# Kernel tuning notes

Measured on AMD Instinct MI355X. Metric: run time of the kernel, lower is better.

## Reference

```python
import jax, jax.numpy as jnp
import numpy as np
from jax.ops import segment_sum

N, E, F_IN, G, C = 20000, 640000, 128, 64, 2


def setup_inputs() -> dict:
    key = jax.random.key(0)
    ks = jax.random.split(key, 16)
    g = lambda k, s: (jax.random.normal(k, s, jnp.float32) * 0.05)
    z = lambda s: jnp.zeros(s, jnp.float32)
    inp = {
        'x': jax.random.normal(ks[0], (N, F_IN), jnp.float32),
        'edge_index': jax.random.randint(ks[1], (2, E), 0, N),
        'batch': jnp.sort(jax.random.randint(ks[2], (N,), 0, G)),
        'w1': g(ks[3], (F_IN, 64)), 'b1': z((64,)),
        'w2': g(ks[4], (64, 64)), 'b2': z((64,)),
        'w3': g(ks[5], (64, 128)), 'b3': z((128,)),
        'w4': g(ks[6], (128, 256)), 'b4': z((256,)),
        'lstm_wih': g(ks[7], (512, 256)), 'lstm_whh': g(ks[8], (512, 128)),
        'lstm_bih': z((512,)), 'lstm_bhh': z((512,)),
        'attn_in_w': g(ks[9], (384, 128)), 'attn_in_b': z((384,)),
        'attn_out_w': g(ks[10], (128, 128)), 'attn_out_b': z((128,)),
        'lin1_w': g(ks[11], (64, 128)), 'lin1_b': z((64,)),
        'lin2_w': g(ks[12], (C, 64)), 'lin2_b': z((C,)),
    }
    return inp


def _gcn(x, src, dst, norm, w, b):
    # PyG GCNConv: h = x @ W; out[dst] += norm_e * h[src]; + bias
    h = x @ w
    msg = h[src] * norm[:, None]
    return segment_sum(msg, dst, num_segments=N) + b


def forward(x, edge_index, batch, w1, b1, w2, b2, w3, b3, w4, b4,
            lstm_wih, lstm_whh, lstm_bih, lstm_bhh,
            attn_in_w, attn_in_b, attn_out_w, attn_out_b,
            lin1_w, lin1_b, lin2_w, lin2_b):
    # ---- GCN normalization with self-loops (shared across layers) ----
    loop = jnp.arange(N)
    src = jnp.concatenate([edge_index[0], loop])
    dst = jnp.concatenate([edge_index[1], loop])
    deg = segment_sum(jnp.ones_like(src, jnp.float32), dst, num_segments=N)
    dinv = jnp.where(deg > 0, jax.lax.rsqrt(deg), 0.0)
    norm = dinv[src] * dinv[dst]

    h = jax.nn.relu(_gcn(x, src, dst, norm, w1, b1))   # [N,64]  (dropout = eval no-op)
    h = jax.nn.relu(_gcn(h, src, dst, norm, w2, b2))   # [N,64]
    h = jax.nn.relu(_gcn(h, src, dst, norm, w3, b3))   # [N,128]
    h = jax.nn.relu(_gcn(h, src, dst, norm, w4, b4))   # [N,256]

    # ---- LSTM over the node sequence (batch 1, seq N), PyTorch gate order i,f,g,o ----
    xg = h @ lstm_wih.T + (lstm_bih + lstm_bhh)        # [N,512] precomputed input gates

    def step(carry, xg_t):
        hh, cc = carry
        gates = xg_t + lstm_whh @ hh                    # [512]
        i, f, gg, o = jnp.split(gates, 4)
        i, f, o = jax.nn.sigmoid(i), jax.nn.sigmoid(f), jax.nn.sigmoid(o)
        cc = f * cc + i * jnp.tanh(gg)
        hh = o * jnp.tanh(cc)
        return (hh, cc), hh

    init = (jnp.zeros(128, h.dtype), jnp.zeros(128, h.dtype))
    _, hs = jax.lax.scan(step, init, xg)               # [N,128]

    # ---- MultiheadAttention: input (L=1, B=N, E=128); softmax over length-1 seq ----
    qkv = hs @ attn_in_w.T + attn_in_b                 # [N,384]
    q, k, v = jnp.split(qkv, 3, axis=-1)
    qh = q.reshape(N, 8, 16); kh = k.reshape(N, 8, 16); vh = v.reshape(N, 8, 16)
    scores = jnp.sum(qh * kh, -1, keepdims=True) / 4.0  # [N,8,1], key dim = 1
    a = jax.nn.softmax(scores, axis=-1)                 # == 1 (single key)
    ctx = (a * vh).reshape(N, 128)
    attn = ctx @ attn_out_w.T + attn_out_b             # [N,128]

    # ---- global mean pool over graphs ----
    sums = segment_sum(attn, batch, num_segments=G)    # [G,128]
    cnt = segment_sum(jnp.ones(N, attn.dtype), batch, num_segments=G)
    pooled = sums / jnp.maximum(cnt, 1.0)[:, None]

    z1 = jax.nn.relu(pooled @ lin1_w.T + lin1_b)
    logits = z1 @ lin2_w.T + lin2_b                    # [G,C]
    return jax.nn.log_softmax(logits, axis=1)


def reference(x, edge_index, batch, w1, b1, w2, b2, w3, b3, w4, b4,
              lstm_wih, lstm_whh, lstm_bih, lstm_bhh,
              attn_in_w, attn_in_b, attn_out_w, attn_out_b,
              lin1_w, lin1_b, lin2_w, lin2_b):
    return forward(x, edge_index, batch, w1, b1, w2, b2, w3, b3, w4, b4,
                   lstm_wih, lstm_whh, lstm_bih, lstm_bhh,
                   attn_in_w, attn_in_b, attn_out_w, attn_out_b,
                   lin1_w, lin1_b, lin2_w, lin2_b)
```

## Files before the change

### kernel.cpp

```cpp
#include <hip/hip_runtime.h>
#include <cstdint>
#include <cstddef>

#define N_NODES 20000
#define N_EDGES 640000
#define N_GRAPH 64

typedef __attribute__((ext_vector_type(8))) short bf16x8;
typedef __attribute__((ext_vector_type(4))) float f32x4;

__device__ __forceinline__ float sigmoidf_(float x) {
    return 1.0f / (1.0f + __expf(-x));
}
__device__ __forceinline__ float tanhf_(float x) {
    float xc = fminf(fmaxf(x, -9.0f), 9.0f);
    float e = __expf(2.0f * xc);
    return (e - 1.0f) / (e + 1.0f);
}
__device__ __forceinline__ unsigned short f2bf_(float x) {
    unsigned int u = __builtin_bit_cast(unsigned int, x);
    return (unsigned short)((u + 0x7fffu + ((u >> 16) & 1u)) >> 16);
}
__device__ __forceinline__ float sel4_(f32x4 v, bool b1, bool b2) {
    float lo = b1 ? v.y : v.x;
    float hi = b1 ? v.w : v.z;
    return b2 ? hi : lo;
}

__global__ void count_kernel(const int* __restrict__ dst, int* __restrict__ cnt, int e) {
    int i = blockIdx.x * blockDim.x + threadIdx.x;
    if (i < e) atomicAdd(&cnt[dst[i]], 1);
}

__global__ void scan_kernel(const int* __restrict__ cnt, int* __restrict__ rowstart, int n) {
    __shared__ int buf[1024];
    __shared__ int carry_sh;
    int tid = threadIdx.x;
    if (tid == 0) carry_sh = 0;
    __syncthreads();
    for (int base = 0; base < n; base += 1024) {
        int i = base + tid;
        int v = (i < n) ? cnt[i] : 0;
        buf[tid] = v;
        __syncthreads();
        for (int off = 1; off < 1024; off <<= 1) {
            int t = (tid >= off) ? buf[tid - off] : 0;
            __syncthreads();
            buf[tid] += t;
            __syncthreads();
        }
        int carry = carry_sh;
        if (i < n) rowstart[i] = carry + buf[tid] - v;
        __syncthreads();
        if (tid == 1023) carry_sh = carry + buf[1023];
        __syncthreads();
    }
    if (tid == 0) rowstart[n] = carry_sh;
}

__global__ void dinv_kernel(const int* __restrict__ cnt, float* __restrict__ dinv, int n) {
    int i = blockIdx.x * blockDim.x + threadIdx.x;
    if (i < n) dinv[i] = rsqrtf((float)cnt[i] + 1.0f);
}

__global__ void fill_kernel(const int* __restrict__ src, const int* __restrict__ dst,
                            const int* __restrict__ rowstart, int* __restrict__ cursor,
                            int* __restrict__ csr_src, int e) {
    int i = blockIdx.x * blockDim.x + threadIdx.x;
    if (i < e) {
        int d = dst[i];
        int pos = rowstart[d] + atomicAdd(&cursor[d], 1);
        csr_src[pos] = src[i];
    }
}

template <bool BT, bool RELU, bool BIAS>
__global__ void gemm_kernel(const float* __restrict__ A, const float* __restrict__ B,
                            const float* __restrict__ bias, float* __restrict__ C,
                            int M, int K, int F) {
    __shared__ float As[16][65];
    __shared__ float Bs[16][65];
    int bm = blockIdx.x * 64;
    int bn = blockIdx.y * 64;
    int tid = threadIdx.x;
    int tm = (tid >> 4) << 2;
    int tn = (tid & 15) << 2;
    float acc[4][4] = {};
    for (int k0 = 0; k0 < K; k0 += 16) {
        {
            int idx = tid * 4;
            int m = idx >> 4;
            int kk = idx & 15;
            int gm = bm + m;
            float4 v = make_float4(0.f, 0.f, 0.f, 0.f);
            if (gm < M) v = *(const float4*)&A[(size_t)gm * K + k0 + kk];
            As[kk + 0][m] = v.x; As[kk + 1][m] = v.y; As[kk + 2][m] = v.z; As[kk + 3][m] = v.w;
        }
        if (BT) {
            int idx = tid * 4;
            int nn = idx >> 4;
            int kk = idx & 15;
            float4 v = *(const float4*)&B[(size_t)(bn + nn) * K + k0 + kk];
            Bs[kk + 0][nn] = v.x; Bs[kk + 1][nn] = v.y; Bs[kk + 2][nn] = v.z; Bs[kk + 3][nn] = v.w;
        } else {
            int idx = tid * 4;
            int kk = idx >> 6;
            int nn = idx & 63;
            float4 v = *(const float4*)&B[(size_t)(k0 + kk) * F + bn + nn];
            Bs[kk][nn + 0] = v.x; Bs[kk][nn + 1] = v.y; Bs[kk][nn + 2] = v.z; Bs[kk][nn + 3] = v.w;
        }
        __syncthreads();
#pragma unroll
        for (int kk = 0; kk < 16; ++kk) {
            float av[4], bv[4];
#pragma unroll
            for (int i = 0; i < 4; ++i) av[i] = As[kk][tm + i];
#pragma unroll
            for (int j = 0; j < 4; ++j) bv[j] = Bs[kk][tn + j];
#pragma unroll
            for (int i = 0; i < 4; ++i)
#pragma unroll
                for (int j = 0; j < 4; ++j) acc[i][j] += av[i] * bv[j];
        }
        __syncthreads();
    }
#pragma unroll
    for (int i = 0; i < 4; ++i) {
        int gm = bm + tm + i;
        if (gm >= M) continue;
#pragma unroll
        for (int j = 0; j < 4; ++j) {
            float v = acc[i][j];
            if (BIAS) v += bias[bn + tn + j];
            if (RELU) v = fmaxf(v, 0.0f);
            C[(size_t)gm * F + bn + tn + j] = v;
        }
    }
}

__global__ void agg_kernel(const float* __restrict__ H, const int* __restrict__ rowstart,
                           const int* __restrict__ csr_src, const float* __restrict__ dinv,
                           const float* __restrict__ bias, float* __restrict__ OUT, int F) {
    int n = blockIdx.x;
    int f = threadIdx.x;
    float di = dinv[n];
    int s = rowstart[n], e = rowstart[n + 1];
    float acc = di * H[(size_t)n * F + f];
    for (int i = s; i < e; ++i) {
        int src = csr_src[i];
        acc += dinv[src] * H[(size_t)src * F + f];
    }
    OUT[(size_t)n * F + f] = fmaxf(bias[f] + di * acc, 0.0f);
}

__global__ void vadd_kernel(const float* __restrict__ a, const float* __restrict__ b,
                            float* __restrict__ o, int n) {
    int i = blockIdx.x * blockDim.x + threadIdx.x;
    if (i < n) o[i] = a[i] + b[i];
}

__global__ void wprep_kernel(const float* __restrict__ whh, uint4* __restrict__ out) {
    int tau = blockIdx.x * blockDim.x + threadIdx.x;
    if (tau >= 8192) return;
    int l  = tau & 63;
    int f  = (tau >> 6) & 15;
    int w  = tau >> 10;
    int s  = f >> 2, kc = f & 3;
    int grow = 128 * s + 16 * w + (l & 15);
    int kb   = kc * 32 + (l >> 4) * 8;
    const float* src = whh + (size_t)grow * 128 + kb;
    unsigned int h[8];
#pragma unroll
    for (int j = 0; j < 8; ++j) h[j] = f2bf_(src[j]);
    uint4 v;
    v.x = h[0] | (h[1] << 16);
    v.y = h[2] | (h[3] << 16);
    v.z = h[4] | (h[5] << 16);
    v.w = h[6] | (h[7] << 16);
    out[tau] = v;
}

#define SF(i, A0, A1, A2, A3) { \
    uint4 q = wfr[(size_t)(w * 16 + (i)) * 64 + l]; \
    asm volatile("v_accvgpr_write_b32 a" #A0 ", %0\n\t" \
                 "v_accvgpr_write_b32 a" #A1 ", %1\n\t" \
                 "v_accvgpr_write_b32 a" #A2 ", %2\n\t" \
                 "v_accvgpr_write_b32 a" #A3 ", %3" \
                 :: "v"(q.x), "v"(q.y), "v"(q.z), "v"(q.w) \
                 : "a" #A0, "a" #A1, "a" #A2, "a" #A3); }

#define LSTM_STEP(N, X0, X1, X2, X3, RD, WR) do { \
    bf16x8 b0 = *(const bf16x8*)&h_bf[RD][ 0 + lg * 8]; \
    bf16x8 b1 = *(const bf16x8*)&h_bf[RD][32 + lg * 8]; \
    bf16x8 b2 = *(const bf16x8*)&h_bf[RD][64 + lg * 8]; \
    bf16x8 b3 = *(const bf16x8*)&h_bf[RD][96 + lg * 8]; \
    asm volatile( \
        "s_nop 1\n\t" \
        "v_mfma_f32_16x16x32_bf16 %0, a[0:3],   %4, %0\n\t" \
        "v_mfma_f32_16x16x32_bf16 %1, a[16:19], %4, %1\n\t" \
        "v_mfma_f32_16x16x32_bf16 %2, a[32:35], %4, %2\n\t" \
        "v_mfma_f32_16x16x32_bf16 %3, a[48:51], %4, %3" \
        : "+v"(X0), "+v"(X1), "+v"(X2), "+v"(X3) : "v"(b0)); \
    asm volatile( \
        "v_mfma_f32_16x16x32_bf16 %0, a[4:7],   %4, %0\n\t" \
        "v_mfma_f32_16x16x32_bf16 %1, a[20:23], %4, %1\n\t" \
        "v_mfma_f32_16x16x32_bf16 %2, a[36:39], %4, %2\n\t" \
        "v_mfma_f32_16x16x32_bf16 %3, a[52:55], %4, %3" \
        : "+v"(X0), "+v"(X1), "+v"(X2), "+v"(X3) : "v"(b1)); \
    asm volatile( \
        "v_mfma_f32_16x16x32_bf16 %0, a[8:11],  %4, %0\n\t" \
        "v_mfma_f32_16x16x32_bf16 %1, a[24:27], %4, %1\n\t" \
        "v_mfma_f32_16x16x32_bf16 %2, a[40:43], %4, %2\n\t" \
        "v_mfma_f32_16x16x32_bf16 %3, a[56:59], %4, %3" \
        : "+v"(X0), "+v"(X1), "+v"(X2), "+v"(X3) : "v"(b2)); \
    asm volatile( \
        "v_mfma_f32_16x16x32_bf16 %0, a[12:15], %4, %0\n\t" \
        "v_mfma_f32_16x16x32_bf16 %1, a[28:31], %4, %1\n\t" \
        "v_mfma_f32_16x16x32_bf16 %2, a[44:47], %4, %2\n\t" \
        "v_mfma_f32_16x16x32_bf16 %3, a[60:63], %4, %3\n\t" \
        "s_nop 7\n\t" \
        "s_nop 7" \
        : "+v"(X0), "+v"(X1), "+v"(X2), "+v"(X3) : "v"(b3)); \
     \
    float gi = sel4_(X0, s1m, s2m); \
    float gf = sel4_(X1, s1m, s2m); \
    float gG = sel4_(X2, s1m, s2m); \
    float go = sel4_(X3, s1m, s2m); \
    { int np = ((N) + 2 < steps) ? (N) + 2 : (N); \
      const float* xp = xg + (size_t)np * 512 + xoff; \
      X0 = *(const f32x4*)(xp); \
      X1 = *(const f32x4*)(xp + 128); \
      X2 = *(const f32x4*)(xp + 256); \
      X3 = *(const f32x4*)(xp + 384); } \
    float iv = sigmoidf_(gi); \
    float fv = sigmoidf_(gf); \
    float gv = tanhf_(gG); \
    float ov = sigmoidf_(go); \
    c = fv * c + iv * gv; \
    float hn = ov * tanhf_(c); \
    if (wrlane) h_bf[WR][uidx] = f2bf_(hn); \
    while ((N) == bnext) { \
        if (wrlane) poolsum[gidx * 128 + uidx] = pacc; \
        pacc = 0.0f; ++gidx; bnext = bnd_s[gidx + 1]; \
    } \
    pacc += hn; \
    asm volatile("s_waitcnt lgkmcnt(0)\n\ts_barrier" ::: "memory"); \
} while (0)

__global__ __launch_bounds__(512)
__attribute__((amdgpu_waves_per_eu(2, 2)))
void lstm_mfma_kernel(const float* __restrict__ xg, const uint4* __restrict__ wfr,
                      const int* __restrict__ batch, float* __restrict__ poolsum, int steps) {
    __shared__ __align__(16) unsigned short h_bf[2][128];
    __shared__ int bnd_s[65];
    const int t = threadIdx.x;
    const int w = t >> 6;
    const int l = t & 63;
    const int lg = l >> 4;
    const bool s1m = (l & 1) != 0;
    const bool s2m = (l & 2) != 0;
    const bool wrlane = (l & 15) < 4;
    const int uidx = 16 * w + 4 * lg + (l & 3);
    const int xoff = 16 * w + 4 * lg;

    SF(0, 0, 1, 2, 3)     SF(1, 4, 5, 6, 7)     SF(2, 8, 9, 10, 11)    SF(3, 12, 13, 14, 15)
    SF(4, 16, 17, 18, 19) SF(5, 20, 21, 22, 23) SF(6, 24, 25, 26, 27)  SF(7, 28, 29, 30, 31)
    SF(8, 32, 33, 34, 35) SF(9, 36, 37, 38, 39) SF(10, 40, 41, 42, 43) SF(11, 44, 45, 46, 47)
    SF(12, 48, 49, 50, 51) SF(13, 52, 53, 54, 55) SF(14, 56, 57, 58, 59) SF(15, 60, 61, 62, 63)

    if (t < 128) h_bf[0][t] = 0;
    if (t <= 64) {
        int lo = 0, hi = steps;
        while (lo < hi) { int m = (lo + hi) >> 1; if (batch[m] < t) lo = m + 1; else hi = m; }
        bnd_s[t] = lo;
    }
    float c = 0.0f, pacc = 0.0f;

    const float* x0p = xg + xoff;
    f32x4 xa0 = *(const f32x4*)(x0p);
    f32x4 xa1 = *(const f32x4*)(x0p + 128);
    f32x4 xa2 = *(const f32x4*)(x0p + 256);
    f32x4 xa3 = *(const f32x4*)(x0p + 384);
    const float* x1p = xg + 512 + xoff;
    f32x4 xb0 = *(const f32x4*)(x1p);
    f32x4 xb1 = *(const f32x4*)(x1p + 128);
    f32x4 xb2 = *(const f32x4*)(x1p + 256);
    f32x4 xb3 = *(const f32x4*)(x1p + 384);
    __syncthreads();
    int gidx = 0, bnext = bnd_s[1];

    for (int n = 0; n < steps; n += 2) {
        LSTM_STEP(n,     xa0, xa1, xa2, xa3, 0, 1);
        LSTM_STEP(n + 1, xb0, xb1, xb2, xb3, 1, 0);
    }
    if (wrlane) poolsum[gidx * 128 + uidx] = pacc;
}

__global__ void head_kernel(const float* __restrict__ poolsum, const int* __restrict__ batch,
                            int nn,
                            const float* __restrict__ attn_in_w, const float* __restrict__ attn_in_b,
                            const float* __restrict__ attn_out_w, const float* __restrict__ attn_out_b,
                            const float* __restrict__ l1w, const float* __restrict__ l1b,
                            const float* __restrict__ l2w, const float* __restrict__ l2b,
                            float* __restrict__ out) {
    __shared__ float hbar[128], tv[128], pl[128], z1[64], lg[2];
    int g = blockIdx.x, t = threadIdx.x;
    int lo = 0, hi = nn;
    while (lo < hi) { int m = (lo + hi) >> 1; if (batch[m] < g) lo = m + 1; else hi = m; }
    int s0 = lo;
    lo = 0; hi = nn;
    while (lo < hi) { int m = (lo + hi) >> 1; if (batch[m] <= g) lo = m + 1; else hi = m; }
    int e0 = lo;
    float cntv = fmaxf((float)(e0 - s0), 1.0f);
    hbar[t] = poolsum[g * 128 + t] / cntv;
    __syncthreads();
    float a = attn_in_b[256 + t];
    for (int k = 0; k < 128; ++k) a += attn_in_w[(256 + t) * 128 + k] * hbar[k];
    tv[t] = a;
    __syncthreads();
    float pv = attn_out_b[t];
    for (int k = 0; k < 128; ++k) pv += attn_out_w[t * 128 + k] * tv[k];
    pl[t] = pv;
    __syncthreads();
    if (t < 64) {
        float z = l1b[t];
        for (int k = 0; k < 128; ++k) z += l1w[t * 128 + k] * pl[k];
        z1[t] = fmaxf(z, 0.0f);
    }
    __syncthreads();
    if (t < 2) {
        float lv = l2b[t];
        for (int k = 0; k < 64; ++k) lv += l2w[t * 64 + k] * z1[k];
        lg[t] = lv;
    }
    __syncthreads();
    if (t == 0) {
        float m = fmaxf(lg[0], lg[1]);
        float ls = m + logf(__expf(lg[0] - m) + __expf(lg[1] - m));
        out[g * 2 + 0] = lg[0] - ls;
        out[g * 2 + 1] = lg[1] - ls;
    }
}

extern "C" void kernel_launch(void* const* d_in, const int* in_sizes, int n_in,
                              void* d_out, int out_size, void* d_ws, size_t ws_size,
                              hipStream_t stream) {
    const float* x          = (const float*)d_in[0];
    const int*   ei         = (const int*)d_in[1];
    const int*   batch      = (const int*)d_in[2];
    const float* w1 = (const float*)d_in[3];  const float* b1 = (const float*)d_in[4];
    const float* w2 = (const float*)d_in[5];  const float* b2 = (const float*)d_in[6];
    const float* w3 = (const float*)d_in[7];  const float* b3 = (const float*)d_in[8];
    const float* w4 = (const float*)d_in[9];  const float* b4 = (const float*)d_in[10];
    const float* wih = (const float*)d_in[11]; const float* whh = (const float*)d_in[12];
    const float* bih = (const float*)d_in[13]; const float* bhh = (const float*)d_in[14];
    const float* attn_in_w  = (const float*)d_in[15]; const float* attn_in_b  = (const float*)d_in[16];
    const float* attn_out_w = (const float*)d_in[17]; const float* attn_out_b = (const float*)d_in[18];
    const float* l1w = (const float*)d_in[19]; const float* l1b = (const float*)d_in[20];
    const float* l2w = (const float*)d_in[21]; const float* l2b = (const float*)d_in[22];
    float* out = (float*)d_out;

    char* p = (char*)d_ws;
    auto alloc = [&](size_t bytes) {
        char* r = p;
        p += (bytes + 255) & ~(size_t)255;
        return r;
    };
    int*   cnt      = (int*)alloc((size_t)N_NODES * 4);
    int*   cursor   = (int*)alloc((size_t)N_NODES * 4);
    int*   rowstart = (int*)alloc((size_t)(N_NODES + 1) * 4);
    float* dinv     = (float*)alloc((size_t)N_NODES * 4);
    int*   csr      = (int*)alloc((size_t)N_EDGES * 4);
    float* bsum     = (float*)alloc(512 * 4);
    float* poolsum  = (float*)alloc((size_t)N_GRAPH * 128 * 4);
    uint4* wfrag    = (uint4*)alloc((size_t)8192 * 16);
    float* bufA     = (float*)alloc((size_t)N_NODES * 256 * 4);
    float* bufB     = (float*)alloc((size_t)N_NODES * 256 * 4);
    float* xg       = (float*)alloc((size_t)N_NODES * 512 * 4);

    hipMemsetAsync(cnt, 0, (size_t)N_NODES * 4, stream);
    hipMemsetAsync(cursor, 0, (size_t)N_NODES * 4, stream);
    hipMemsetAsync(poolsum, 0, (size_t)N_GRAPH * 128 * 4, stream);

    const int* srcp = ei;
    const int* dstp = ei + N_EDGES;

    int eb = (N_EDGES + 255) / 256;
    int nb = (N_NODES + 255) / 256;
    count_kernel<<<eb, 256, 0, stream>>>(dstp, cnt, N_EDGES);
    scan_kernel<<<1, 1024, 0, stream>>>(cnt, rowstart, N_NODES);
    dinv_kernel<<<nb, 256, 0, stream>>>(cnt, dinv, N_NODES);
    fill_kernel<<<eb, 256, 0, stream>>>(srcp, dstp, rowstart, cursor, csr, N_EDGES);
    wprep_kernel<<<32, 256, 0, stream>>>(whh, wfrag);

    int mg = (N_NODES + 63) / 64;
    gemm_kernel<false, false, false><<<dim3(mg, 1), 256, 0, stream>>>(x, w1, nullptr, bufA, N_NODES, 128, 64);
    agg_kernel<<<N_NODES, 64, 0, stream>>>(bufA, rowstart, csr, dinv, b1, bufB, 64);
    gemm_kernel<false, false, false><<<dim3(mg, 1), 256, 0, stream>>>(bufB, w2, nullptr, bufA, N_NODES, 64, 64);
    agg_kernel<<<N_NODES, 64, 0, stream>>>(bufA, rowstart, csr, dinv, b2, bufB, 64);
    gemm_kernel<false, false, false><<<dim3(mg, 2), 256, 0, stream>>>(bufB, w3, nullptr, bufA, N_NODES, 64, 128);
    agg_kernel<<<N_NODES, 128, 0, stream>>>(bufA, rowstart, csr, dinv, b3, bufB, 128);
    gemm_kernel<false, false, false><<<dim3(mg, 4), 256, 0, stream>>>(bufB, w4, nullptr, bufA, N_NODES, 128, 256);
    agg_kernel<<<N_NODES, 256, 0, stream>>>(bufA, rowstart, csr, dinv, b4, bufB, 256);

    vadd_kernel<<<2, 256, 0, stream>>>(bih, bhh, bsum, 512);
    gemm_kernel<true, false, true><<<dim3(mg, 8), 256, 0, stream>>>(bufB, wih, bsum, xg, N_NODES, 256, 512);

    lstm_mfma_kernel<<<1, 512, 0, stream>>>(xg, (const uint4*)wfrag, batch, poolsum, N_NODES);

    head_kernel<<<N_GRAPH, 128, 0, stream>>>(poolsum, batch, N_NODES,
                                             attn_in_w, attn_in_b, attn_out_w, attn_out_b,
                                             l1w, l1b, l2w, l2b, out);
}
```

Measured before the change: 12.67 ms.

## Halve LSTM workgroup to 4 waves, each computing 32 hidden units

The sequential LSTM kernel now runs with 4 waves instead of 8. Each wave holds twice as many W_hh bf16 fragments in AGPRs (128 AGPRs) and issues 8 MFMAs per k-chunk covering 32 hidden units. The weight prep layout and the xg prefetch are reworked to match. The aim is to cut per-step barrier cost and wave-count overhead on the serial recurrence. In exchange, each wave does twice the MFMA and activation work per step, which lengthens the critical path within a wave and raises register pressure.

```diff
diff --git a/kernel.cpp b/kernel.cpp
--- a/kernel.cpp
+++ b/kernel.cpp
@@ -163,25 +163,28 @@
     int tau = blockIdx.x * blockDim.x + threadIdx.x;
     if (tau >= 8192) return;
     int l  = tau & 63;
-    int f  = (tau >> 6) & 15;
-    int w  = tau >> 10;
-    int s  = f >> 2, kc = f & 3;
-    int grow = 128 * s + 16 * w + (l & 15);
+    int i  = (tau >> 6) & 31;
+    int w  = tau >> 11;
+    int kc = i & 3;
+    int sh = i >> 2;
+    int h  = sh & 1;
+    int s  = sh >> 1;
+    int grow = 128 * s + 32 * w + 16 * h + (l & 15);
     int kb   = kc * 32 + (l >> 4) * 8;
     const float* src = whh + (size_t)grow * 128 + kb;
-    unsigned int h[8];
-#pragma unroll
-    for (int j = 0; j < 8; ++j) h[j] = f2bf_(src[j]);
+    unsigned int hv[8];
+#pragma unroll
+    for (int j = 0; j < 8; ++j) hv[j] = f2bf_(src[j]);
     uint4 v;
-    v.x = h[0] | (h[1] << 16);
-    v.y = h[2] | (h[3] << 16);
-    v.z = h[4] | (h[5] << 16);
-    v.w = h[6] | (h[7] << 16);
+    v.x = hv[0] | (hv[1] << 16);
+    v.y = hv[2] | (hv[3] << 16);
+    v.z = hv[4] | (hv[5] << 16);
+    v.w = hv[6] | (hv[7] << 16);
     out[tau] = v;
 }
 
 #define SF(i, A0, A1, A2, A3) { \
-    uint4 q = wfr[(size_t)(w * 16 + (i)) * 64 + l]; \
+    uint4 q = wfr[(size_t)(w * 32 + (i)) * 64 + l]; \
     asm volatile("v_accvgpr_write_b32 a" #A0 ", %0\n\t" \
                  "v_accvgpr_write_b32 a" #A1 ", %1\n\t" \
                  "v_accvgpr_write_b32 a" #A2 ", %2\n\t" \
@@ -189,66 +192,88 @@
                  :: "v"(q.x), "v"(q.y), "v"(q.z), "v"(q.w) \
                  : "a" #A0, "a" #A1, "a" #A2, "a" #A3); }
 
-#define LSTM_STEP(N, X0, X1, X2, X3, RD, WR) do { \
+#define LSTM_STEP(N, X00, X01, X10, X11, X20, X21, X30, X31, RD, WR) do { \
     bf16x8 b0 = *(const bf16x8*)&h_bf[RD][ 0 + lg * 8]; \
     bf16x8 b1 = *(const bf16x8*)&h_bf[RD][32 + lg * 8]; \
     bf16x8 b2 = *(const bf16x8*)&h_bf[RD][64 + lg * 8]; \
     bf16x8 b3 = *(const bf16x8*)&h_bf[RD][96 + lg * 8]; \
     asm volatile( \
         "s_nop 1\n\t" \
-        "v_mfma_f32_16x16x32_bf16 %0, a[0:3],   %4, %0\n\t" \
-        "v_mfma_f32_16x16x32_bf16 %1, a[16:19], %4, %1\n\t" \
-        "v_mfma_f32_16x16x32_bf16 %2, a[32:35], %4, %2\n\t" \
-        "v_mfma_f32_16x16x32_bf16 %3, a[48:51], %4, %3" \
-        : "+v"(X0), "+v"(X1), "+v"(X2), "+v"(X3) : "v"(b0)); \
+        "v_mfma_f32_16x16x32_bf16 %0, a[0:3],     %8, %0\n\t" \
+        "v_mfma_f32_16x16x32_bf16 %1, a[16:19],   %8, %1\n\t" \
+        "v_mfma_f32_16x16x32_bf16 %2, a[32:35],   %8, %2\n\t" \
+        "v_mfma_f32_16x16x32_bf16 %3, a[48:51],   %8, %3\n\t" \
+        "v_mfma_f32_16x16x32_bf16 %4, a[64:67],   %8, %4\n\t" \
+        "v_mfma_f32_16x16x32_bf16 %5, a[80:83],   %8, %5\n\t" \
+        "v_mfma_f32_16x16x32_bf16 %6, a[96:99],   %8, %6\n\t" \
+        "v_mfma_f32_16x16x32_bf16 %7, a[112:115], %8, %7" \
+        : "+v"(X00), "+v"(X01), "+v"(X10), "+v"(X11), \
+          "+v"(X20), "+v"(X21), "+v"(X30), "+v"(X31) : "v"(b0)); \
     asm volatile( \
-        "v_mfma_f32_16x16x32_bf16 %0, a[4:7],   %4, %0\n\t" \
-        "v_mfma_f32_16x16x32_bf16 %1, a[20:23], %4, %1\n\t" \
-        "v_mfma_f32_16x16x32_bf16 %2, a[36:39], %4, %2\n\t" \
-        "v_mfma_f32_16x16x32_bf16 %3, a[52:55], %4, %3" \
-        : "+v"(X0), "+v"(X1), "+v"(X2), "+v"(X3) : "v"(b1)); \
+        "v_mfma_f32_16x16x32_bf16 %0, a[4:7],     %8, %0\n\t" \
+        "v_mfma_f32_16x16x32_bf16 %1, a[20:23],   %8, %1\n\t" \
+        "v_mfma_f32_16x16x32_bf16 %2, a[36:39],   %8, %2\n\t" \
+        "v_mfma_f32_16x16x32_bf16 %3, a[52:55],   %8, %3\n\t" \
+        "v_mfma_f32_16x16x32_bf16 %4, a[68:71],   %8, %4\n\t" \
+        "v_mfma_f32_16x16x32_bf16 %5, a[84:87],   %8, %5\n\t" \
+        "v_mfma_f32_16x16x32_bf16 %6, a[100:103], %8, %6\n\t" \
+        "v_mfma_f32_16x16x32_bf16 %7, a[116:119], %8, %7" \
+        : "+v"(X00), "+v"(X01), "+v"(X10), "+v"(X11), \
+          "+v"(X20), "+v"(X21), "+v"(X30), "+v"(X31) : "v"(b1)); \
     asm volatile( \
-        "v_mfma_f32_16x16x32_bf16 %0, a[8:11],  %4, %0\n\t" \
-        "v_mfma_f32_16x16x32_bf16 %1, a[24:27], %4, %1\n\t" \
-        "v_mfma_f32_16x16x32_bf16 %2, a[40:43], %4, %2\n\t" \
-        "v_mfma_f32_16x16x32_bf16 %3, a[56:59], %4, %3" \
-        : "+v"(X0), "+v"(X1), "+v"(X2), "+v"(X3) : "v"(b2)); \
+        "v_mfma_f32_16x16x32_bf16 %0, a[8:11],    %8, %0\n\t" \
+        "v_mfma_f32_16x16x32_bf16 %1, a[24:27],   %8, %1\n\t" \
+        "v_mfma_f32_16x16x32_bf16 %2, a[40:43],   %8, %2\n\t" \
+        "v_mfma_f32_16x16x32_bf16 %3, a[56:59],   %8, %3\n\t" \
+        "v_mfma_f32_16x16x32_bf16 %4, a[72:75],   %8, %4\n\t" \
+        "v_mfma_f32_16x16x32_bf16 %5, a[88:91],   %8, %5\n\t" \
+        "v_mfma_f32_16x16x32_bf16 %6, a[104:107], %8, %6\n\t" \
+        "v_mfma_f32_16x16x32_bf16 %7, a[120:123], %8, %7" \
+        : "+v"(X00), "+v"(X01), "+v"(X10), "+v"(X11), \
+          "+v"(X20), "+v"(X21), "+v"(X30), "+v"(X31) : "v"(b2)); \
     asm volatile( \
-        "v_mfma_f32_16x16x32_bf16 %0, a[12:15], %4, %0\n\t" \
-        "v_mfma_f32_16x16x32_bf16 %1, a[28:31], %4, %1\n\t" \
-        "v_mfma_f32_16x16x32_bf16 %2, a[44:47], %4, %2\n\t" \
-        "v_mfma_f32_16x16x32_bf16 %3, a[60:63], %4, %3\n\t" \
+        "v_mfma_f32_16x16x32_bf16 %0, a[12:15],   %8, %0\n\t" \
+        "v_mfma_f32_16x16x32_bf16 %1, a[28:31],   %8, %1\n\t" \
+        "v_mfma_f32_16x16x32_bf16 %2, a[44:47],   %8, %2\n\t" \
+        "v_mfma_f32_16x16x32_bf16 %3, a[60:63],   %8, %3\n\t" \
+        "v_mfma_f32_16x16x32_bf16 %4, a[76:79],   %8, %4\n\t" \
+        "v_mfma_f32_16x16x32_bf16 %5, a[92:95],   %8, %5\n\t" \
+        "v_mfma_f32_16x16x32_bf16 %6, a[108:111], %8, %6\n\t" \
+        "v_mfma_f32_16x16x32_bf16 %7, a[124:127], %8, %7\n\t" \
         "s_nop 7\n\t" \
         "s_nop 7" \
-        : "+v"(X0), "+v"(X1), "+v"(X2), "+v"(X3) : "v"(b3)); \
+        : "+v"(X00), "+v"(X01), "+v"(X10), "+v"(X11), \
+          "+v"(X20), "+v"(X21), "+v"(X30), "+v"(X31) : "v"(b3)); \
      \
-    float gi = sel4_(X0, s1m, s2m); \
-    float gf = sel4_(X1, s1m, s2m); \
-    float gG = sel4_(X2, s1m, s2m); \
-    float go = sel4_(X3, s1m, s2m); \
+    float gi0 = sel4_(X00, s1m, s2m), gi1 = sel4_(X01, s1m, s2m); \
+    float gf0 = sel4_(X10, s1m, s2m), gf1 = sel4_(X11, s1m, s2m); \
+    float gg0 = sel4_(X20, s1m, s2m), gg1 = sel4_(X21, s1m, s2m); \
+    float go0 = sel4_(X30, s1m, s2m), go1 = sel4_(X31, s1m, s2m); \
     { int np = ((N) + 2 < steps) ? (N) + 2 : (N); \
-      const float* xp = xg + (size_t)np * 512 + xoff; \
-      X0 = *(const f32x4*)(xp); \
-      X1 = *(const f32x4*)(xp + 128); \
-      X2 = *(const f32x4*)(xp + 256); \
-      X3 = *(const f32x4*)(xp + 384); } \
-    float iv = sigmoidf_(gi); \
-    float fv = sigmoidf_(gf); \
-    float gv = tanhf_(gG); \
-    float ov = sigmoidf_(go); \
-    c = fv * c + iv * gv; \
-    float hn = ov * tanhf_(c); \
-    if (wrlane) h_bf[WR][uidx] = f2bf_(hn); \
+      const float* xp = xg + (size_t)np * 512 + xbase; \
+      X00 = *(const f32x4*)(xp);       X01 = *(const f32x4*)(xp + 16); \
+      X10 = *(const f32x4*)(xp + 128); X11 = *(const f32x4*)(xp + 144); \
+      X20 = *(const f32x4*)(xp + 256); X21 = *(const f32x4*)(xp + 272); \
+      X30 = *(const f32x4*)(xp + 384); X31 = *(const f32x4*)(xp + 400); } \
+    float iv0 = sigmoidf_(gi0), iv1 = sigmoidf_(gi1); \
+    float fv0 = sigmoidf_(gf0), fv1 = sigmoidf_(gf1); \
+    float gv0 = tanhf_(gg0),    gv1 = tanhf_(gg1); \
+    float ov0 = sigmoidf_(go0), ov1 = sigmoidf_(go1); \
+    c0 = fv0 * c0 + iv0 * gv0; \
+    c1 = fv1 * c1 + iv1 * gv1; \
+    float hn0 = ov0 * tanhf_(c0); \
+    float hn1 = ov1 * tanhf_(c1); \
+    if (wrlane) { h_bf[WR][u0] = f2bf_(hn0); h_bf[WR][u1] = f2bf_(hn1); } \
     while ((N) == bnext) { \
-        if (wrlane) poolsum[gidx * 128 + uidx] = pacc; \
-        pacc = 0.0f; ++gidx; bnext = bnd_s[gidx + 1]; \
+        if (wrlane) { poolsum[gidx * 128 + u0] = pacc0; poolsum[gidx * 128 + u1] = pacc1; } \
+        pacc0 = 0.0f; pacc1 = 0.0f; ++gidx; bnext = bnd_s[gidx + 1]; \
     } \
-    pacc += hn; \
+    pacc0 += hn0; pacc1 += hn1; \
     asm volatile("s_waitcnt lgkmcnt(0)\n\ts_barrier" ::: "memory"); \
 } while (0)
 
-__global__ __launch_bounds__(512)
-__attribute__((amdgpu_waves_per_eu(2, 2)))
+__global__ __launch_bounds__(256)
+__attribute__((amdgpu_waves_per_eu(1, 1)))
 void lstm_mfma_kernel(const float* __restrict__ xg, const uint4* __restrict__ wfr,
                       const int* __restrict__ batch, float* __restrict__ poolsum, int steps) {
     __shared__ __align__(16) unsigned short h_bf[2][128];
@@ -260,13 +285,18 @@
     const bool s1m = (l & 1) != 0;
     const bool s2m = (l & 2) != 0;
     const bool wrlane = (l & 15) < 4;
-    const int uidx = 16 * w + 4 * lg + (l & 3);
-    const int xoff = 16 * w + 4 * lg;
-
-    SF(0, 0, 1, 2, 3)     SF(1, 4, 5, 6, 7)     SF(2, 8, 9, 10, 11)    SF(3, 12, 13, 14, 15)
-    SF(4, 16, 17, 18, 19) SF(5, 20, 21, 22, 23) SF(6, 24, 25, 26, 27)  SF(7, 28, 29, 30, 31)
-    SF(8, 32, 33, 34, 35) SF(9, 36, 37, 38, 39) SF(10, 40, 41, 42, 43) SF(11, 44, 45, 46, 47)
-    SF(12, 48, 49, 50, 51) SF(13, 52, 53, 54, 55) SF(14, 56, 57, 58, 59) SF(15, 60, 61, 62, 63)
+    const int u0 = 32 * w + 4 * lg + (l & 3);
+    const int u1 = u0 + 16;
+    const int xbase = 32 * w + 4 * lg;
+
+    SF(0, 0, 1, 2, 3)       SF(1, 4, 5, 6, 7)       SF(2, 8, 9, 10, 11)     SF(3, 12, 13, 14, 15)
+    SF(4, 16, 17, 18, 19)   SF(5, 20, 21, 22, 23)   SF(6, 24, 25, 26, 27)   SF(7, 28, 29, 30, 31)
+    SF(8, 32, 33, 34, 35)   SF(9, 36, 37, 38, 39)   SF(10, 40, 41, 42, 43)  SF(11, 44, 45, 46, 47)
+    SF(12, 48, 49, 50, 51)  SF(13, 52, 53, 54, 55)  SF(14, 56, 57, 58, 59)  SF(15, 60, 61, 62, 63)
+    SF(16, 64, 65, 66, 67)  SF(17, 68, 69, 70, 71)  SF(18, 72, 73, 74, 75)  SF(19, 76, 77, 78, 79)
+    SF(20, 80, 81, 82, 83)  SF(21, 84, 85, 86, 87)  SF(22, 88, 89, 90, 91)  SF(23, 92, 93, 94, 95)
+    SF(24, 96, 97, 98, 99)  SF(25, 100, 101, 102, 103) SF(26, 104, 105, 106, 107) SF(27, 108, 109, 110, 111)
+    SF(28, 112, 113, 114, 115) SF(29, 116, 117, 118, 119) SF(30, 120, 121, 122, 123) SF(31, 124, 125, 126, 127)
 
     if (t < 128) h_bf[0][t] = 0;
     if (t <= 64) {
@@ -274,26 +304,26 @@
         while (lo < hi) { int m = (lo + hi) >> 1; if (batch[m] < t) lo = m + 1; else hi = m; }
         bnd_s[t] = lo;
     }
-    float c = 0.0f, pacc = 0.0f;
-
-    const float* x0p = xg + xoff;
-    f32x4 xa0 = *(const f32x4*)(x0p);
-    f32x4 xa1 = *(const f32x4*)(x0p + 128);
-    f32x4 xa2 = *(const f32x4*)(x0p + 256);
-    f32x4 xa3 = *(const f32x4*)(x0p + 384);
-    const float* x1p = xg + 512 + xoff;
-    f32x4 xb0 = *(const f32x4*)(x1p);
-    f32x4 xb1 = *(const f32x4*)(x1p + 128);
-    f32x4 xb2 = *(const f32x4*)(x1p + 256);
-    f32x4 xb3 = *(const f32x4*)(x1p + 384);
+    float c0 = 0.0f, c1 = 0.0f, pacc0 = 0.0f, pacc1 = 0.0f;
+
+    const float* x0p = xg + xbase;
+    f32x4 xa00 = *(const f32x4*)(x0p);       f32x4 xa01 = *(const f32x4*)(x0p + 16);
+    f32x4 xa10 = *(const f32x4*)(x0p + 128); f32x4 xa11 = *(const f32x4*)(x0p + 144);
+    f32x4 xa20 = *(const f32x4*)(x0p + 256); f32x4 xa21 = *(const f32x4*)(x0p + 272);
+    f32x4 xa30 = *(const f32x4*)(x0p + 384); f32x4 xa31 = *(const f32x4*)(x0p + 400);
+    const float* x1p = xg + 512 + xbase;
+    f32x4 xb00 = *(const f32x4*)(x1p);       f32x4 xb01 = *(const f32x4*)(x1p + 16);
+    f32x4 xb10 = *(const f32x4*)(x1p + 128); f32x4 xb11 = *(const f32x4*)(x1p + 144);
+    f32x4 xb20 = *(const f32x4*)(x1p + 256); f32x4 xb21 = *(const f32x4*)(x1p + 272);
+    f32x4 xb30 = *(const f32x4*)(x1p + 384); f32x4 xb31 = *(const f32x4*)(x1p + 400);
     __syncthreads();
     int gidx = 0, bnext = bnd_s[1];
 
     for (int n = 0; n < steps; n += 2) {
-        LSTM_STEP(n,     xa0, xa1, xa2, xa3, 0, 1);
-        LSTM_STEP(n + 1, xb0, xb1, xb2, xb3, 1, 0);
-    }
-    if (wrlane) poolsum[gidx * 128 + uidx] = pacc;
+        LSTM_STEP(n,     xa00, xa01, xa10, xa11, xa20, xa21, xa30, xa31, 0, 1);
+        LSTM_STEP(n + 1, xb00, xb01, xb10, xb11, xb20, xb21, xb30, xb31, 1, 0);
+    }
+    if (wrlane) { poolsum[gidx * 128 + u0] = pacc0; poolsum[gidx * 128 + u1] = pacc1; }
 }
 
 __global__ void head_kernel(const float* __restrict__ poolsum, const int* __restrict__ batch,
@@ -406,7 +436,7 @@
     vadd_kernel<<<2, 256, 0, stream>>>(bih, bhh, bsum, 512);
     gemm_kernel<true, false, true><<<dim3(mg, 8), 256, 0, stream>>>(bufB, wih, bsum, xg, N_NODES, 256, 512);
 
-    lstm_mfma_kernel<<<1, 512, 0, stream>>>(xg, (const uint4*)wfrag, batch, poolsum, N_NODES);
+    lstm_mfma_kernel<<<1, 256, 0, stream>>>(xg, (const uint4*)wfrag, batch, poolsum, N_NODES);
 
     head_kernel<<<N_GRAPH, 128, 0, stream>>>(poolsum, batch, N_NODES,
                                              attn_in_w, attn_in_b, attn_out_w, attn_out_b,
```

New measurement: 17.50 ms. 38.1% more time.
